# Kernel tuning notes

Hardware: AMD Instinct MI355X
Metric: run time of the kernel (lower is better)

Reference implementation:

```python
import jax, jax.numpy as jnp
import numpy as np


def setup_inputs() -> dict:
    key = jax.random.key(0)
    ks = jax.random.split(key, 10)
    N, E, F = 20000, 320000, 128
    q = jax.random.normal(ks[0], (N, F), dtype=jnp.float32)
    mu = jax.random.normal(ks[1], (N, 3, F), dtype=jnp.float32)
    W_ij = jax.random.normal(ks[2], (E, 3 * F), dtype=jnp.float32)
    dir_ij = jax.random.normal(ks[3], (E, 3), dtype=jnp.float32)
    # unit displacement vectors
    dir_ij = dir_ij / jnp.linalg.norm(dir_ij, axis=-1, keepdims=True)
    W1 = jax.random.normal(ks[4], (F, F), dtype=jnp.float32) * (1.0 / np.sqrt(F))
    b1 = jax.random.normal(ks[5], (F,), dtype=jnp.float32) * 0.01
    W2 = jax.random.normal(ks[6], (F, 3 * F), dtype=jnp.float32) * (1.0 / np.sqrt(F))
    b2 = jax.random.normal(ks[7], (3 * F,), dtype=jnp.float32) * 0.01
    idx_i = jax.random.randint(ks[8], (E,), 0, N, dtype=jnp.int64 if jax.config.jax_enable_x64 else jnp.int32)
    idx_j = jax.random.randint(ks[9], (E,), 0, N, dtype=jnp.int64 if jax.config.jax_enable_x64 else jnp.int32)
    return {"q": q, "mu": mu, "W_ij": W_ij, "dir_ij": dir_ij,
            "W1": W1, "b1": b1, "W2": W2, "b2": b2,
            "idx_i": idx_i, "idx_j": idx_j, "n_atoms": N}


def reference(q, mu, W_ij, dir_ij, W1, b1, W2, b2, idx_i, idx_j, n_atoms):
    Fdim = q.shape[-1]
    # context_net: Linear(F,F) -> SiLU -> Linear(F,3F), computed per node [N,3F]
    ctx = jax.nn.silu(q @ W1 + b1) @ W2 + b2
    # gather by source node, elementwise filter: [E,3F]
    x = W_ij * ctx[idx_j]
    dq, dmu_r, dmu_mu = jnp.split(x, 3, axis=-1)  # each [E,F]
    # scatter-add scalar messages to nodes [N,F]
    dq = jax.ops.segment_sum(dq, idx_i, num_segments=n_atoms)
    # vector messages: [E,3,F]
    dmu = dmu_r[:, None, :] * dir_ij[:, :, None] + dmu_mu[:, None, :] * mu[idx_j]
    dmu = jax.ops.segment_sum(dmu, idx_i, num_segments=n_atoms)
    return (q + dq, mu + dmu)
```

## Files before the change

kernel.cpp:

```cpp
#include <hip/hip_runtime.h>


typedef float f2 __attribute__((ext_vector_type(2)));

static __host__ __device__ inline size_t ws_align(size_t x) { return (x + 255) & ~(size_t)255; }

template <bool SILU>
__global__ __launch_bounds__(256, 2) void gemm_bias_act_kernel(
    const float* __restrict__ A, const float* __restrict__ B,
    const float* __restrict__ bias, float* __restrict__ C,
    int M, int Ncols)
{
    __shared__ float As[128][68];
    __shared__ float Bs[128][68];

    const int t    = threadIdx.x;
    const int row0 = blockIdx.x * 64;
    const int col0 = blockIdx.y * 64;

    #pragma unroll
    for (int it = 0; it < 8; ++it) {
        int l    = t + 256 * it;
        int r    = l >> 5;
        int k4   = (l & 31) << 2;
        int grow = row0 + r;
        float4 v = make_float4(0.f, 0.f, 0.f, 0.f);
        if (grow < M) v = *reinterpret_cast<const float4*>(A + (size_t)grow * 128 + k4);
        As[k4 + 0][r] = v.x; As[k4 + 1][r] = v.y;
        As[k4 + 2][r] = v.z; As[k4 + 3][r] = v.w;
    }
    #pragma unroll
    for (int it = 0; it < 8; ++it) {
        int l  = t + 256 * it;
        int k  = l >> 4;
        int c4 = (l & 15) << 2;
        float4 v = *reinterpret_cast<const float4*>(B + (size_t)k * Ncols + col0 + c4);
        *reinterpret_cast<float4*>(&Bs[k][c4]) = v;
    }
    __syncthreads();

    const int tx = t & 15, ty = t >> 4;
    float acc[4][4];
    #pragma unroll
    for (int i = 0; i < 4; ++i)
        #pragma unroll
        for (int j = 0; j < 4; ++j) acc[i][j] = 0.f;

    #pragma unroll 4
    for (int k = 0; k < 128; ++k) {
        float4 a = *reinterpret_cast<const float4*>(&As[k][ty * 4]);
        float4 b = *reinterpret_cast<const float4*>(&Bs[k][tx * 4]);
        acc[0][0] += a.x * b.x; acc[0][1] += a.x * b.y; acc[0][2] += a.x * b.z; acc[0][3] += a.x * b.w;
        acc[1][0] += a.y * b.x; acc[1][1] += a.y * b.y; acc[1][2] += a.y * b.z; acc[1][3] += a.y * b.w;
        acc[2][0] += a.z * b.x; acc[2][1] += a.z * b.y; acc[2][2] += a.z * b.z; acc[2][3] += a.z * b.w;
        acc[3][0] += a.w * b.x; acc[3][1] += a.w * b.y; acc[3][2] += a.w * b.z; acc[3][3] += a.w * b.w;
    }

    float4 bv = *reinterpret_cast<const float4*>(bias + col0 + tx * 4);
    #pragma unroll
    for (int i = 0; i < 4; ++i) {
        int grow = row0 + ty * 4 + i;
        if (grow >= M) continue;
        float4 o;
        o.x = acc[i][0] + bv.x; o.y = acc[i][1] + bv.y;
        o.z = acc[i][2] + bv.z; o.w = acc[i][3] + bv.w;
        if (SILU) {
            o.x = o.x / (1.f + __expf(-o.x));
            o.y = o.y / (1.f + __expf(-o.y));
            o.z = o.z / (1.f + __expf(-o.z));
            o.w = o.w / (1.f + __expf(-o.w));
        }
        *reinterpret_cast<float4*>(C + (size_t)grow * Ncols + col0 + tx * 4) = o;
    }
}

__global__ void zero_int_kernel(int* __restrict__ p, int n) {
    int i = blockIdx.x * 256 + threadIdx.x;
    if (i < n) p[i] = 0;
}

__global__ void count_kernel(const int* __restrict__ idx_i, int* __restrict__ cnt, int E) {
    int e = blockIdx.x * 256 + threadIdx.x;
    if (e < E) atomicAdd(&cnt[idx_i[e]], 1);
}

__global__ __launch_bounds__(256) void scan_kernel(int* __restrict__ cnt_cursor,
                                                   int* __restrict__ row_ptr, int N) {
    __shared__ int sums[256];
    __shared__ int offs[256];
    int t = threadIdx.x;
    int chunk = (N + 255) / 256;
    int lo = t * chunk;
    int hi = lo + chunk; if (hi > N) hi = N; if (lo > N) lo = N;
    int s = 0;
    for (int i = lo; i < hi; ++i) s += cnt_cursor[i];
    sums[t] = s;
    __syncthreads();
    if (t == 0) {
        int acc = 0;
        for (int k = 0; k < 256; ++k) { int v = sums[k]; offs[k] = acc; acc += v; }
    }
    __syncthreads();
    int acc = offs[t];
    for (int i = lo; i < hi; ++i) {
        int v = cnt_cursor[i];
        cnt_cursor[i] = acc;
        row_ptr[i]    = acc;
        acc += v;
    }
    if (t == 255) row_ptr[N] = acc;
}

__global__ void fill_kernel(const int* __restrict__ idx_i, const int* __restrict__ idx_j,
                            int* __restrict__ cursor, int2* __restrict__ payload, int E) {
    int e = blockIdx.x * 256 + threadIdx.x;
    if (e < E) {
        int pos = atomicAdd(&cursor[idx_i[e]], 1);
        payload[pos] = make_int2(e, idx_j[e]);
    }
}

__global__ __launch_bounds__(256) void node_kernel(
    const float* __restrict__ q, const float* __restrict__ mu,
    const float* __restrict__ ctx, const float* __restrict__ W_ij,
    const float* __restrict__ dir_ij, const int* __restrict__ row_ptr,
    const int2* __restrict__ payload, float* __restrict__ out, int N)
{
    int wid  = (blockIdx.x * blockDim.x + threadIdx.x) >> 6;
    int lane = threadIdx.x & 63;
    if (wid >= N) return;

    int p   = row_ptr[wid];
    int end = row_ptr[wid + 1];
    const int f = lane * 2;

    f2 qa  = {0.f, 0.f};
    f2 ma0 = {0.f, 0.f}, ma1 = {0.f, 0.f}, ma2 = {0.f, 0.f};

    while (p + 4 <= end) {
        int2 pl[4];
        #pragma unroll
        for (int u = 0; u < 4; ++u) pl[u] = payload[p + u];

        f2 wq[4], wr[4], wm[4], cq[4], cr[4], cm[4], m0[4], m1[4], m2[4];
        float d0[4], d1[4], d2[4];
        #pragma unroll
        for (int u = 0; u < 4; ++u) {
            const float* w  = W_ij + (size_t)pl[u].x * 384;
            const float* cj = ctx  + (size_t)pl[u].y * 384;
            const float* mj = mu   + (size_t)pl[u].y * 384;
            wq[u] = __builtin_nontemporal_load(reinterpret_cast<const f2*>(w + f));
            wr[u] = __builtin_nontemporal_load(reinterpret_cast<const f2*>(w + 128 + f));
            wm[u] = __builtin_nontemporal_load(reinterpret_cast<const f2*>(w + 256 + f));
            cq[u] = *reinterpret_cast<const f2*>(cj + f);
            cr[u] = *reinterpret_cast<const f2*>(cj + 128 + f);
            cm[u] = *reinterpret_cast<const f2*>(cj + 256 + f);
            m0[u] = *reinterpret_cast<const f2*>(mj + f);
            m1[u] = *reinterpret_cast<const f2*>(mj + 128 + f);
            m2[u] = *reinterpret_cast<const f2*>(mj + 256 + f);
            d0[u] = __builtin_nontemporal_load(dir_ij + 3 * (size_t)pl[u].x + 0);
            d1[u] = __builtin_nontemporal_load(dir_ij + 3 * (size_t)pl[u].x + 1);
            d2[u] = __builtin_nontemporal_load(dir_ij + 3 * (size_t)pl[u].x + 2);
        }
        #pragma unroll
        for (int u = 0; u < 4; ++u) {
            qa += wq[u] * cq[u];
            f2 xr = wr[u] * cr[u];
            f2 xm = wm[u] * cm[u];
            ma0 += xr * d0[u] + xm * m0[u];
            ma1 += xr * d1[u] + xm * m1[u];
            ma2 += xr * d2[u] + xm * m2[u];
        }
        p += 4;
    }
    while (p < end) {
        int2 pl = payload[p++];
        const float* w  = W_ij + (size_t)pl.x * 384;
        const float* cj = ctx  + (size_t)pl.y * 384;
        const float* mj = mu   + (size_t)pl.y * 384;
        f2 wq = __builtin_nontemporal_load(reinterpret_cast<const f2*>(w + f));
        f2 wr = __builtin_nontemporal_load(reinterpret_cast<const f2*>(w + 128 + f));
        f2 wm = __builtin_nontemporal_load(reinterpret_cast<const f2*>(w + 256 + f));
        f2 cq = *reinterpret_cast<const f2*>(cj + f);
        f2 cr = *reinterpret_cast<const f2*>(cj + 128 + f);
        f2 cm = *reinterpret_cast<const f2*>(cj + 256 + f);
        f2 m0 = *reinterpret_cast<const f2*>(mj + f);
        f2 m1 = *reinterpret_cast<const f2*>(mj + 128 + f);
        f2 m2 = *reinterpret_cast<const f2*>(mj + 256 + f);
        float d0 = __builtin_nontemporal_load(dir_ij + 3 * (size_t)pl.x + 0);
        float d1 = __builtin_nontemporal_load(dir_ij + 3 * (size_t)pl.x + 1);
        float d2 = __builtin_nontemporal_load(dir_ij + 3 * (size_t)pl.x + 2);
        qa += wq * cq;
        f2 xr = wr * cr;
        f2 xm = wm * cm;
        ma0 += xr * d0 + xm * m0;
        ma1 += xr * d1 + xm * m1;
        ma2 += xr * d2 + xm * m2;
    }

    f2 qv = __builtin_nontemporal_load(reinterpret_cast<const f2*>(q + (size_t)wid * 128 + f));
    __builtin_nontemporal_store(qv + qa, reinterpret_cast<f2*>(out + (size_t)wid * 128 + f));

    const float* mbase = mu + (size_t)wid * 384;
    float* obase = out + (size_t)N * 128 + (size_t)wid * 384;
    f2 mv0 = *reinterpret_cast<const f2*>(mbase + f);
    f2 mv1 = *reinterpret_cast<const f2*>(mbase + 128 + f);
    f2 mv2 = *reinterpret_cast<const f2*>(mbase + 256 + f);
    __builtin_nontemporal_store(mv0 + ma0, reinterpret_cast<f2*>(obase + f));
    __builtin_nontemporal_store(mv1 + ma1, reinterpret_cast<f2*>(obase + 128 + f));
    __builtin_nontemporal_store(mv2 + ma2, reinterpret_cast<f2*>(obase + 256 + f));
}

extern "C" void kernel_launch(void* const* d_in, const int* in_sizes, int n_in,
                              void* d_out, int out_size, void* d_ws, size_t ws_size,
                              hipStream_t stream) {
    const float* q      = (const float*)d_in[0];
    const float* mu     = (const float*)d_in[1];
    const float* W_ij   = (const float*)d_in[2];
    const float* dir_ij = (const float*)d_in[3];
    const float* W1     = (const float*)d_in[4];
    const float* b1     = (const float*)d_in[5];
    const float* W2     = (const float*)d_in[6];
    const float* b2     = (const float*)d_in[7];
    const int*   idx_i  = (const int*)d_in[8];
    const int*   idx_j  = (const int*)d_in[9];

    const int N = in_sizes[0] / 128;
    const int E = in_sizes[8];
    float* out = (float*)d_out;

    char* ws = (char*)d_ws;
    size_t off = 0;
    float* ctx     = (float*)(ws + off); off += ws_align((size_t)N * 384 * 4);
    float* h       = (float*)(ws + off); off += ws_align((size_t)N * 128 * 4);
    int*   row_ptr = (int*)  (ws + off); off += ws_align((size_t)(N + 1) * 4);
    int*   cursor  = (int*)  (ws + off); off += ws_align((size_t)N * 4);
    int2*  payload = (int2*) (ws + off); off += ws_align((size_t)E * 8);
    (void)ws_size; (void)n_in; (void)out_size;

    const int nblk_rows = (N + 63) / 64;
    const int eblk = (E + 255) / 256;
    const int nblk = (N + 255) / 256;

    gemm_bias_act_kernel<true ><<<dim3(nblk_rows, 2), 256, 0, stream>>>(q, W1, b1, h,   N, 128);
    gemm_bias_act_kernel<false><<<dim3(nblk_rows, 6), 256, 0, stream>>>(h, W2, b2, ctx, N, 384);

    zero_int_kernel<<<nblk, 256, 0, stream>>>(cursor, N);
    count_kernel<<<eblk, 256, 0, stream>>>(idx_i, cursor, E);
    scan_kernel<<<1, 256, 0, stream>>>(cursor, row_ptr, N);
    fill_kernel<<<eblk, 256, 0, stream>>>(idx_i, idx_j, cursor, payload, E);

    node_kernel<<<(N + 3) / 4, 256, 0, stream>>>(q, mu, ctx, W_ij, dir_ij,
                                                 row_ptr, payload, out, N);
}
```

Baseline: 919.4 us.

## Split wavefront into half-waves using float4 loads, reduce halves via shuffle

The node kernel now has each half of a 64-lane wavefront process a different edge. Each lane uses 16-byte float4 loads over 128 features instead of 8-byte float2 loads. The two halves' partial sums are combined with cross-lane XOR shuffles, and the final q/mu writes are split between the halves. Occupancy is also hinted at 3 blocks per CU. This is meant to widen memory transactions and keep more independent gathers in flight, at the cost of extra shuffles and idle lanes on odd-degree tails.

Measured after the change: 918.4 us. Within noise of the previous version (-0.1%).

```diff
diff --git a/kernel.cpp b/kernel.cpp
--- a/kernel.cpp
+++ b/kernel.cpp
@@ -1,7 +1,7 @@
 #include <hip/hip_runtime.h>
 
 
-typedef float f2 __attribute__((ext_vector_type(2)));
+typedef float f4 __attribute__((ext_vector_type(4)));
 
 static __host__ __device__ inline size_t ws_align(size_t x) { return (x + 255) & ~(size_t)255; }
 
@@ -120,7 +120,43 @@
     }
 }
 
-__global__ __launch_bounds__(256) void node_kernel(
+struct EdgeRegs { f4 wq, wr, wm, cq, cr, cm, m0, m1, m2; float d0, d1, d2; };
+
+__device__ __forceinline__ EdgeRegs load_edge(
+    const float* __restrict__ W_ij, const float* __restrict__ ctx,
+    const float* __restrict__ mu, const float* __restrict__ dir_ij,
+    int2 pl, int fb)
+{
+    EdgeRegs r;
+    const float* w  = W_ij + (size_t)pl.x * 384 + fb;
+    const float* cj = ctx  + (size_t)pl.y * 384 + fb;
+    const float* mj = mu   + (size_t)pl.y * 384 + fb;
+    const float* dp = dir_ij + 3 * (size_t)pl.x;
+    r.wq = __builtin_nontemporal_load(reinterpret_cast<const f4*>(w));
+    r.wr = __builtin_nontemporal_load(reinterpret_cast<const f4*>(w + 128));
+    r.wm = __builtin_nontemporal_load(reinterpret_cast<const f4*>(w + 256));
+    r.cq = *reinterpret_cast<const f4*>(cj);
+    r.cr = *reinterpret_cast<const f4*>(cj + 128);
+    r.cm = *reinterpret_cast<const f4*>(cj + 256);
+    r.m0 = *reinterpret_cast<const f4*>(mj);
+    r.m1 = *reinterpret_cast<const f4*>(mj + 128);
+    r.m2 = *reinterpret_cast<const f4*>(mj + 256);
+    r.d0 = __builtin_nontemporal_load(dp + 0);
+    r.d1 = __builtin_nontemporal_load(dp + 1);
+    r.d2 = __builtin_nontemporal_load(dp + 2);
+    return r;
+}
+
+__device__ __forceinline__ void accum(const EdgeRegs& r, f4& qa, f4& ma0, f4& ma1, f4& ma2) {
+    qa += r.wq * r.cq;
+    f4 xr = r.wr * r.cr;
+    f4 xm = r.wm * r.cm;
+    ma0 += xr * r.d0 + xm * r.m0;
+    ma1 += xr * r.d1 + xm * r.m1;
+    ma2 += xr * r.d2 + xm * r.m2;
+}
+
+__global__ __launch_bounds__(256, 3) void node_kernel(
     const float* __restrict__ q, const float* __restrict__ mu,
     const float* __restrict__ ctx, const float* __restrict__ W_ij,
     const float* __restrict__ dir_ij, const int* __restrict__ row_ptr,
@@ -132,83 +168,57 @@
 
     int p   = row_ptr[wid];
     int end = row_ptr[wid + 1];
-    const int f = lane * 2;
-
-    f2 qa  = {0.f, 0.f};
-    f2 ma0 = {0.f, 0.f}, ma1 = {0.f, 0.f}, ma2 = {0.f, 0.f};
+    const int half = lane >> 5;
+    const int fb   = (lane & 31) << 2;
+
+    f4 qa  = {0.f, 0.f, 0.f, 0.f};
+    f4 ma0 = qa, ma1 = qa, ma2 = qa;
 
     while (p + 4 <= end) {
-        int2 pl[4];
-        #pragma unroll
-        for (int u = 0; u < 4; ++u) pl[u] = payload[p + u];
-
-        f2 wq[4], wr[4], wm[4], cq[4], cr[4], cm[4], m0[4], m1[4], m2[4];
-        float d0[4], d1[4], d2[4];
-        #pragma unroll
-        for (int u = 0; u < 4; ++u) {
-            const float* w  = W_ij + (size_t)pl[u].x * 384;
-            const float* cj = ctx  + (size_t)pl[u].y * 384;
-            const float* mj = mu   + (size_t)pl[u].y * 384;
-            wq[u] = __builtin_nontemporal_load(reinterpret_cast<const f2*>(w + f));
-            wr[u] = __builtin_nontemporal_load(reinterpret_cast<const f2*>(w + 128 + f));
-            wm[u] = __builtin_nontemporal_load(reinterpret_cast<const f2*>(w + 256 + f));
-            cq[u] = *reinterpret_cast<const f2*>(cj + f);
-            cr[u] = *reinterpret_cast<const f2*>(cj + 128 + f);
-            cm[u] = *reinterpret_cast<const f2*>(cj + 256 + f);
-            m0[u] = *reinterpret_cast<const f2*>(mj + f);
-            m1[u] = *reinterpret_cast<const f2*>(mj + 128 + f);
-            m2[u] = *reinterpret_cast<const f2*>(mj + 256 + f);
-            d0[u] = __builtin_nontemporal_load(dir_ij + 3 * (size_t)pl[u].x + 0);
-            d1[u] = __builtin_nontemporal_load(dir_ij + 3 * (size_t)pl[u].x + 1);
-            d2[u] = __builtin_nontemporal_load(dir_ij + 3 * (size_t)pl[u].x + 2);
-        }
-        #pragma unroll
-        for (int u = 0; u < 4; ++u) {
-            qa += wq[u] * cq[u];
-            f2 xr = wr[u] * cr[u];
-            f2 xm = wm[u] * cm[u];
-            ma0 += xr * d0[u] + xm * m0[u];
-            ma1 += xr * d1[u] + xm * m1[u];
-            ma2 += xr * d2[u] + xm * m2[u];
-        }
+        int2 pl0 = payload[p + half];
+        int2 pl1 = payload[p + 2 + half];
+        EdgeRegs r0 = load_edge(W_ij, ctx, mu, dir_ij, pl0, fb);
+        EdgeRegs r1 = load_edge(W_ij, ctx, mu, dir_ij, pl1, fb);
+        accum(r0, qa, ma0, ma1, ma2);
+        accum(r1, qa, ma0, ma1, ma2);
         p += 4;
     }
-    while (p < end) {
-        int2 pl = payload[p++];
-        const float* w  = W_ij + (size_t)pl.x * 384;
-        const float* cj = ctx  + (size_t)pl.y * 384;
-        const float* mj = mu   + (size_t)pl.y * 384;
-        f2 wq = __builtin_nontemporal_load(reinterpret_cast<const f2*>(w + f));
-        f2 wr = __builtin_nontemporal_load(reinterpret_cast<const f2*>(w + 128 + f));
-        f2 wm = __builtin_nontemporal_load(reinterpret_cast<const f2*>(w + 256 + f));
-        f2 cq = *reinterpret_cast<const f2*>(cj + f);
-        f2 cr = *reinterpret_cast<const f2*>(cj + 128 + f);
-        f2 cm = *reinterpret_cast<const f2*>(cj + 256 + f);
-        f2 m0 = *reinterpret_cast<const f2*>(mj + f);
-        f2 m1 = *reinterpret_cast<const f2*>(mj + 128 + f);
-        f2 m2 = *reinterpret_cast<const f2*>(mj + 256 + f);
-        float d0 = __builtin_nontemporal_load(dir_ij + 3 * (size_t)pl.x + 0);
-        float d1 = __builtin_nontemporal_load(dir_ij + 3 * (size_t)pl.x + 1);
-        float d2 = __builtin_nontemporal_load(dir_ij + 3 * (size_t)pl.x + 2);
-        qa += wq * cq;
-        f2 xr = wr * cr;
-        f2 xm = wm * cm;
-        ma0 += xr * d0 + xm * m0;
-        ma1 += xr * d1 + xm * m1;
-        ma2 += xr * d2 + xm * m2;
-    }
-
-    f2 qv = __builtin_nontemporal_load(reinterpret_cast<const f2*>(q + (size_t)wid * 128 + f));
-    __builtin_nontemporal_store(qv + qa, reinterpret_cast<f2*>(out + (size_t)wid * 128 + f));
-
-    const float* mbase = mu + (size_t)wid * 384;
+    if (p + 2 <= end) {
+        int2 pl = payload[p + half];
+        EdgeRegs r = load_edge(W_ij, ctx, mu, dir_ij, pl, fb);
+        accum(r, qa, ma0, ma1, ma2);
+        p += 2;
+    }
+    if (p < end && half == 0) {
+        int2 pl = payload[p];
+        EdgeRegs r = load_edge(W_ij, ctx, mu, dir_ij, pl, fb);
+        accum(r, qa, ma0, ma1, ma2);
+    }
+
+    #pragma unroll
+    for (int c = 0; c < 4; ++c) {
+        qa[c]  += __shfl_xor(qa[c],  32);
+        ma0[c] += __shfl_xor(ma0[c], 32);
+        ma1[c] += __shfl_xor(ma1[c], 32);
+        ma2[c] += __shfl_xor(ma2[c], 32);
+    }
+
+    const float* mbase = mu  + (size_t)wid * 384;
+    const float* qrow  = q   + (size_t)wid * 128;
     float* obase = out + (size_t)N * 128 + (size_t)wid * 384;
-    f2 mv0 = *reinterpret_cast<const f2*>(mbase + f);
-    f2 mv1 = *reinterpret_cast<const f2*>(mbase + 128 + f);
-    f2 mv2 = *reinterpret_cast<const f2*>(mbase + 256 + f);
-    __builtin_nontemporal_store(mv0 + ma0, reinterpret_cast<f2*>(obase + f));
-    __builtin_nontemporal_store(mv1 + ma1, reinterpret_cast<f2*>(obase + 128 + f));
-    __builtin_nontemporal_store(mv2 + ma2, reinterpret_cast<f2*>(obase + 256 + f));
+    float* oqrow = out + (size_t)wid * 128;
+
+    const float* inA = half ? mbase         : qrow;
+    const float* inB = half ? (mbase + 256) : (mbase + 128);
+    float*       oA  = half ? obase         : oqrow;
+    float*       oB  = half ? (obase + 256) : (obase + 128);
+    f4 sA = half ? ma0 : qa;
+    f4 sB = half ? ma2 : ma1;
+
+    f4 vA = *reinterpret_cast<const f4*>(inA + fb);
+    f4 vB = *reinterpret_cast<const f4*>(inB + fb);
+    __builtin_nontemporal_store(vA + sA, reinterpret_cast<f4*>(oA + fb));
+    __builtin_nontemporal_store(vB + sB, reinterpret_cast<f4*>(oB + fb));
 }
 
 extern "C" void kernel_launch(void* const* d_in, const int* in_sizes, int n_in,
```
